# Performance work log

Measured on AMD Instinct MI355X. Metric: run time of the kernel, lower is better.

Reference implementation:

```python
import jax, jax.numpy as jnp
import numpy as np

NUM_TOPICS = 100
VOCAB = 8192
MC_N = 20
MD_N = 20
LAMBDA_D = 0.7
LAMBDA_A = 100.0
WARMUP_RATIO = 0.5
NUM_EPOCHS = 200


def setup_inputs() -> dict:
    key = jax.random.key(0)
    k1, k2 = jax.random.split(key)
    beta = jax.random.normal(k1, (NUM_TOPICS, VOCAB), dtype=jnp.float32)
    W = jax.random.uniform(k2, (VOCAB, VOCAB), dtype=jnp.float32)
    # fill_diagonal_(1) in __init__
    d = jnp.arange(VOCAB)
    W = W.at[d, d].set(1.0)
    return {"beta": beta, "coherence_weight": W, "epoch": 120}


def reference(beta, coherence_weight, epoch):
    K, V = beta.shape
    rows = jnp.arange(K)[:, None]

    # --- Mc: top-Mc_n mask -> additive -99999 on non-topk entries ---
    _, mc_idx = jax.lax.top_k(beta, MC_N)                      # [K, Mc_n]
    Mc = jnp.zeros_like(beta).at[rows, mc_idx].set(1.0)        # [K, V]
    Mc_add = (1.0 - Mc) * (-99999.0)

    # softmax over masked beta is detached in the original
    p = jax.lax.stop_gradient(jax.nn.softmax(beta + Mc_add, axis=1))
    M = p @ coherence_weight                                    # [K, V]

    # row-wise min-max normalize, then Wc = 1 - normalized
    m_min = jnp.min(M, axis=1, keepdims=True)
    m_max = jnp.max(M, axis=1, keepdims=True)
    Wc = 1.0 - (M - m_min) / (m_max - m_min)

    loss = 100.0 * jax.nn.softmax(beta, axis=1) ** 2 * Wc       # [K, V]

    # --- diversity mask Md (lambda_d > 0.5 branch) ---
    _, md_idx = jax.lax.top_k(beta, MD_N)
    Md_mask = jnp.zeros_like(beta).at[rows, md_idx].set(1.0)    # [K, V]
    # Md[t, v] = any other row has v in its top-Md_n
    col_sum = jnp.sum(Md_mask, axis=0)                          # [V]
    Md = (col_sum[None, :] - Md_mask) > 0                       # [K, V] bool

    pos = jnp.sum(jnp.where(Md, loss, 0.0))
    neg = jnp.sum(jnp.where(Md, 0.0, loss))
    total = (pos * LAMBDA_D + neg * (1.0 - LAMBDA_D)) * 2.0

    warmup_epochs = int(WARMUP_RATIO * NUM_EPOCHS)              # 100
    lambda_a_delta = LAMBDA_A / warmup_epochs
    lambda_a = epoch * lambda_a_delta if epoch < warmup_epochs else LAMBDA_A
    return lambda_a * total
```

## Files before the change

kernel.cpp:

```cpp
#include <hip/hip_runtime.h>
#include <math.h>

#define NT 100
#define VOCAB 8192
#define TOPN 20
#define CHUNKS 8
#define CCOLS (VOCAB / CHUNKS)
#define CAP 4096

__global__ __launch_bounds__(256) void topk_kernel(
    const float* __restrict__ beta,
    int*   __restrict__ top_idx,
    float* __restrict__ top_p,
    float* __restrict__ rowstats)
{
    const int k = blockIdx.x;
    const int t = threadIdx.x;

    __shared__ float srow[VOCAB];
    __shared__ float sred[4];
    __shared__ int   sredi[4];
    __shared__ float s_T;
    __shared__ int   s_base;
    __shared__ float cu[CAP];
    __shared__ unsigned short ci[CAP];
    __shared__ float s_winv[TOPN];
    __shared__ int   s_wini[TOPN];
    __shared__ float s_ps;

    const float* row = beta + (size_t)k * VOCAB;

    float mx = -INFINITY;
#pragma unroll
    for (int i = 0; i < VOCAB / (256 * 4); ++i) {
        float4 v = *reinterpret_cast<const float4*>(row + (size_t)(i * 256 + t) * 4);
        reinterpret_cast<float4*>(srow)[i * 256 + t] = v;
        mx = fmaxf(mx, fmaxf(fmaxf(v.x, v.y), fmaxf(v.z, v.w)));
    }
#pragma unroll
    for (int off = 32; off >= 1; off >>= 1) mx = fmaxf(mx, __shfl_down(mx, off));
    if ((t & 63) == 0) sred[t >> 6] = mx;
    __syncthreads();
    const float rowmax = fmaxf(fmaxf(sred[0], sred[1]), fmaxf(sred[2], sred[3]));

    float T = rowmax - 2.0f;
    for (int guard = 0; guard < 64; ++guard) {
        int c = 0;
#pragma unroll
        for (int i = 0; i < VOCAB / 256; ++i) c += (srow[i * 256 + t] >= T) ? 1 : 0;
#pragma unroll
        for (int off = 32; off >= 1; off >>= 1) c += __shfl_down(c, off);
        if ((t & 63) == 0) sredi[t >> 6] = c;
        __syncthreads();
        const int cnt = sredi[0] + sredi[1] + sredi[2] + sredi[3];
        if (cnt >= TOPN) { if (t == 0) s_T = T; break; }
        T -= 0.5f;
        __syncthreads();
    }
    if (t == 0) s_base = 0;
    __syncthreads();
    T = s_T;

#pragma unroll
    for (int i = 0; i < VOCAB / 256; ++i) {
        const int idx = i * 256 + t;
        const float v = srow[idx];
        const bool pr = (v >= T);
        const unsigned long long mask = __ballot(pr);
        const int lane = t & 63;
        const int pre = __popcll(mask & ((1ull << lane) - 1ull));
        const int nb  = __popcll(mask);
        int base = 0;
        if (lane == 0 && nb) base = atomicAdd(&s_base, nb);
        base = __shfl(base, 0);
        if (pr) {
            const int p = base + pre;
            if (p < CAP) { cu[p] = v; ci[p] = (unsigned short)idx; }
        }
    }
    __syncthreads();
    const int ncand = min(s_base, CAP);

    if (t < 64) {
        for (int it = 0; it < TOPN; ++it) {
            float bv = -INFINITY; int bp = -1;
            for (int p = t; p < ncand; p += 64) {
                const float v = cu[p];
                if (v > bv) { bv = v; bp = p; }
            }
#pragma unroll
            for (int off = 32; off >= 1; off >>= 1) {
                const float ov = __shfl_down(bv, off);
                const int   op = __shfl_down(bp, off);
                if (ov > bv) { bv = ov; bp = op; }
            }
            bp = __shfl(bp, 0);
            bv = __shfl(bv, 0);
            if (t == 0) { s_winv[it] = bv; s_wini[it] = ci[bp]; }
            cu[bp] = -INFINITY;
        }
    }
    __syncthreads();

    if (t == 0) {
        float ps = 0.f;
#pragma unroll
        for (int j = 0; j < TOPN; ++j) ps += expf(s_winv[j] - rowmax);
        s_ps = ps;
    }
    __syncthreads();
    if (t < TOPN) {
        top_idx[k * TOPN + t] = s_wini[t];
        top_p[k * TOPN + t]   = expf(s_winv[t] - rowmax) / s_ps;
    }

    float se = 0.f;
#pragma unroll
    for (int i = 0; i < VOCAB / 256; ++i) se += expf(srow[i * 256 + t] - rowmax);
#pragma unroll
    for (int off = 32; off >= 1; off >>= 1) se += __shfl_down(se, off);
    if ((t & 63) == 0) sred[t >> 6] = se;
    __syncthreads();
    if (t == 0) {
        rowstats[2 * k + 0] = rowmax;
        rowstats[2 * k + 1] = sred[0] + sred[1] + sred[2] + sred[3];
    }
}

__global__ __launch_bounds__(256) void mcompute_kernel(
    const float* __restrict__ W,
    const int*   __restrict__ top_idx,
    const float* __restrict__ top_p,
    float* __restrict__ M,
    float* __restrict__ mmpart)
{
    const int b = blockIdx.x;
    const int k = b / CHUNKS;
    const int c = b % CHUNKS;
    const int t = threadIdx.x;

    __shared__ int   sIdx[TOPN];
    __shared__ float sP[TOPN];
    __shared__ float sA[4], sB[4];
    if (t < TOPN) { sIdx[t] = top_idx[k * TOPN + t]; sP[t] = top_p[k * TOPN + t]; }
    __syncthreads();

    int   idx_r[TOPN];
    float p_r[TOPN];
#pragma unroll
    for (int j = 0; j < TOPN; ++j) { idx_r[j] = sIdx[j]; p_r[j] = sP[j]; }

    const int col = c * CCOLS + t * 4;
    float4 m = make_float4(0.f, 0.f, 0.f, 0.f);
#pragma unroll
    for (int j = 0; j < TOPN; ++j) {
        const float4 w = *reinterpret_cast<const float4*>(W + (size_t)idx_r[j] * VOCAB + col);
        const float pj = p_r[j];
        m.x += pj * w.x; m.y += pj * w.y; m.z += pj * w.z; m.w += pj * w.w;
    }
    *reinterpret_cast<float4*>(M + (size_t)k * VOCAB + col) = m;

    float mn = fminf(fminf(m.x, m.y), fminf(m.z, m.w));
    float mxv = fmaxf(fmaxf(m.x, m.y), fmaxf(m.z, m.w));
#pragma unroll
    for (int off = 32; off >= 1; off >>= 1) {
        mn  = fminf(mn,  __shfl_down(mn,  off));
        mxv = fmaxf(mxv, __shfl_down(mxv, off));
    }
    if ((t & 63) == 0) { sA[t >> 6] = mn; sB[t >> 6] = mxv; }
    __syncthreads();
    if (t == 0) {
        mmpart[(k * CHUNKS + c) * 2 + 0] = fminf(fminf(sA[0], sA[1]), fminf(sA[2], sA[3]));
        mmpart[(k * CHUNKS + c) * 2 + 1] = fmaxf(fmaxf(sB[0], sB[1]), fmaxf(sB[2], sB[3]));
    }
}

__global__ __launch_bounds__(1024) void loss_kernel(
    const float* __restrict__ beta,
    const float* __restrict__ M,
    const int*   __restrict__ top_idx,
    const float* __restrict__ rowstats,
    const float* __restrict__ mmpart,
    float* __restrict__ posk,
    float* __restrict__ negk)
{
    const int k = blockIdx.x;
    const int t = threadIdx.x;

    __shared__ int cnt[VOCAB];
    __shared__ float sredA[16], sredB[16];
    __shared__ float s_mn, s_mx;

#pragma unroll
    for (int i = 0; i < VOCAB / 1024; ++i) cnt[i * 1024 + t] = 0;
    __syncthreads();

    for (int e = t; e < NT * TOPN; e += 1024) atomicAdd(&cnt[top_idx[e]], 1);
    __syncthreads();
    if (t < TOPN) atomicSub(&cnt[top_idx[k * TOPN + t]], 1);
    if (t == 0) {
        float mn = INFINITY, mxv = -INFINITY;
        for (int c = 0; c < CHUNKS; ++c) {
            mn  = fminf(mn,  mmpart[(k * CHUNKS + c) * 2 + 0]);
            mxv = fmaxf(mxv, mmpart[(k * CHUNKS + c) * 2 + 1]);
        }
        s_mn = mn; s_mx = mxv;
    }
    __syncthreads();

    const float mmin = s_mn;
    const float inv  = 1.0f / (s_mx - mmin);
    const float rmax = rowstats[2 * k + 0];
    const float rinv = 1.0f / rowstats[2 * k + 1];

    float pos = 0.f, neg = 0.f;
#pragma unroll
    for (int i = 0; i < VOCAB / (1024 * 4); ++i) {
        const int v = (i * 1024 + t) * 4;
        const float4 m = *reinterpret_cast<const float4*>(M + (size_t)k * VOCAB + v);
        const float4 b = *reinterpret_cast<const float4*>(beta + (size_t)k * VOCAB + v);
        {
            const float Wc = 1.0f - (m.x - mmin) * inv;
            const float sb = expf(b.x - rmax) * rinv;
            const float l  = 100.f * sb * sb * Wc;
            if (cnt[v + 0] > 0) pos += l; else neg += l;
        }
        {
            const float Wc = 1.0f - (m.y - mmin) * inv;
            const float sb = expf(b.y - rmax) * rinv;
            const float l  = 100.f * sb * sb * Wc;
            if (cnt[v + 1] > 0) pos += l; else neg += l;
        }
        {
            const float Wc = 1.0f - (m.z - mmin) * inv;
            const float sb = expf(b.z - rmax) * rinv;
            const float l  = 100.f * sb * sb * Wc;
            if (cnt[v + 2] > 0) pos += l; else neg += l;
        }
        {
            const float Wc = 1.0f - (m.w - mmin) * inv;
            const float sb = expf(b.w - rmax) * rinv;
            const float l  = 100.f * sb * sb * Wc;
            if (cnt[v + 3] > 0) pos += l; else neg += l;
        }
    }
#pragma unroll
    for (int off = 32; off >= 1; off >>= 1) {
        pos += __shfl_down(pos, off);
        neg += __shfl_down(neg, off);
    }
    if ((t & 63) == 0) { sredA[t >> 6] = pos; sredB[t >> 6] = neg; }
    __syncthreads();
    if (t == 0) {
        float a = 0.f, b2 = 0.f;
        for (int w = 0; w < 16; ++w) { a += sredA[w]; b2 += sredB[w]; }
        posk[k] = a;
        negk[k] = b2;
    }
}

__global__ void finalize_kernel(const float* __restrict__ posk,
                                const float* __restrict__ negk,
                                const int*   __restrict__ epoch,
                                float* __restrict__ out)
{
    if (threadIdx.x == 0 && blockIdx.x == 0) {
        float pos = 0.f, neg = 0.f;
        for (int i = 0; i < NT; ++i) { pos += posk[i]; neg += negk[i]; }
        const float total = (pos * 0.7f + neg * 0.3f) * 2.0f;
        const int e = *epoch;
        const float la = (e < 100) ? (float)e : 100.0f;
        *out = la * total;
    }
}

extern "C" void kernel_launch(void* const* d_in, const int* in_sizes, int n_in,
                              void* d_out, int out_size, void* d_ws, size_t ws_size,
                              hipStream_t stream)
{
    (void)in_sizes; (void)n_in; (void)out_size; (void)ws_size;
    const float* beta  = (const float*)d_in[0];
    const float* W     = (const float*)d_in[1];
    const int*   epoch = (const int*)d_in[2];
    float* out = (float*)d_out;

    char* ws = (char*)d_ws;
    int*   top_idx  = (int*)ws;    ws += NT * TOPN * sizeof(int);
    float* top_p    = (float*)ws;  ws += NT * TOPN * sizeof(float);
    float* rowstats = (float*)ws;  ws += NT * 2 * sizeof(float);
    float* mmpart   = (float*)ws;  ws += NT * CHUNKS * 2 * sizeof(float);
    float* posk     = (float*)ws;  ws += NT * sizeof(float);
    float* negk     = (float*)ws;  ws += NT * sizeof(float);
    ws = (char*)(((size_t)ws + 255) & ~(size_t)255);
    float* M        = (float*)ws;  ws += (size_t)NT * VOCAB * sizeof(float);

    topk_kernel<<<NT, 256, 0, stream>>>(beta, top_idx, top_p, rowstats);
    mcompute_kernel<<<NT * CHUNKS, 256, 0, stream>>>(W, top_idx, top_p, M, mmpart);
    loss_kernel<<<NT, 1024, 0, stream>>>(beta, M, top_idx, rowstats, mmpart, posk, negk);
    finalize_kernel<<<1, 64, 0, stream>>>(posk, negk, epoch, out);
}
```

Baseline: 56.59 us.

## Fuse M computation with loss via algebraic min-max decomposition

The loss is expanded algebraically into per-chunk sums of w and w*M, so the M matrix never goes to global memory and the separate loss kernel is removed. The min-max normalization is applied later in the finalize kernel. The top-k kernel now keeps the beta row in registers instead of shared memory. This removes one launch and a 3.2MB write/read round trip, but each block now rebuilds a partial histogram of top indices, and the expanded form may lose some floating-point precision.

```diff
diff --git a/kernel.cpp b/kernel.cpp
--- a/kernel.cpp
+++ b/kernel.cpp
@@ -17,7 +17,6 @@
     const int k = blockIdx.x;
     const int t = threadIdx.x;
 
-    __shared__ float srow[VOCAB];
     __shared__ float sred[4];
     __shared__ int   sredi[4];
     __shared__ float s_T;
@@ -30,12 +29,12 @@
 
     const float* row = beta + (size_t)k * VOCAB;
 
+    float4 r[8];
     float mx = -INFINITY;
 #pragma unroll
-    for (int i = 0; i < VOCAB / (256 * 4); ++i) {
-        float4 v = *reinterpret_cast<const float4*>(row + (size_t)(i * 256 + t) * 4);
-        reinterpret_cast<float4*>(srow)[i * 256 + t] = v;
-        mx = fmaxf(mx, fmaxf(fmaxf(v.x, v.y), fmaxf(v.z, v.w)));
+    for (int i = 0; i < 8; ++i) {
+        r[i] = *reinterpret_cast<const float4*>(row + (size_t)(i * 256 + t) * 4);
+        mx = fmaxf(mx, fmaxf(fmaxf(r[i].x, r[i].y), fmaxf(r[i].z, r[i].w)));
     }
 #pragma unroll
     for (int off = 32; off >= 1; off >>= 1) mx = fmaxf(mx, __shfl_down(mx, off));
@@ -47,7 +46,12 @@
     for (int guard = 0; guard < 64; ++guard) {
         int c = 0;
 #pragma unroll
-        for (int i = 0; i < VOCAB / 256; ++i) c += (srow[i * 256 + t] >= T) ? 1 : 0;
+        for (int i = 0; i < 8; ++i) {
+            c += (r[i].x >= T) ? 1 : 0;
+            c += (r[i].y >= T) ? 1 : 0;
+            c += (r[i].z >= T) ? 1 : 0;
+            c += (r[i].w >= T) ? 1 : 0;
+        }
 #pragma unroll
         for (int off = 32; off >= 1; off >>= 1) c += __shfl_down(c, off);
         if ((t & 63) == 0) sredi[t >> 6] = c;
@@ -62,20 +66,22 @@
     T = s_T;
 
 #pragma unroll
-    for (int i = 0; i < VOCAB / 256; ++i) {
-        const int idx = i * 256 + t;
-        const float v = srow[idx];
-        const bool pr = (v >= T);
-        const unsigned long long mask = __ballot(pr);
-        const int lane = t & 63;
-        const int pre = __popcll(mask & ((1ull << lane) - 1ull));
-        const int nb  = __popcll(mask);
-        int base = 0;
-        if (lane == 0 && nb) base = atomicAdd(&s_base, nb);
-        base = __shfl(base, 0);
-        if (pr) {
-            const int p = base + pre;
-            if (p < CAP) { cu[p] = v; ci[p] = (unsigned short)idx; }
+    for (int i = 0; i < 8; ++i) {
+#pragma unroll
+        for (int e = 0; e < 4; ++e) {
+            const float v = (&r[i].x)[e];
+            const int idx = (i * 256 + t) * 4 + e;
+            const bool pr = (v >= T);
+            const unsigned long long mask = __ballot(pr);
+            const int lane = t & 63;
+            const int pre = __popcll(mask & ((1ull << lane) - 1ull));
+            int base = 0;
+            if (lane == 0) base = atomicAdd(&s_base, __popcll(mask));
+            base = __shfl(base, 0);
+            if (pr) {
+                const int p = base + pre;
+                if (p < CAP) { cu[p] = v; ci[p] = (unsigned short)idx; }
+            }
         }
     }
     __syncthreads();
@@ -116,7 +122,12 @@
 
     float se = 0.f;
 #pragma unroll
-    for (int i = 0; i < VOCAB / 256; ++i) se += expf(srow[i * 256 + t] - rowmax);
+    for (int i = 0; i < 8; ++i) {
+        se += expf(r[i].x - rowmax);
+        se += expf(r[i].y - rowmax);
+        se += expf(r[i].z - rowmax);
+        se += expf(r[i].w - rowmax);
+    }
 #pragma unroll
     for (int off = 32; off >= 1; off >>= 1) se += __shfl_down(se, off);
     if ((t & 63) == 0) sred[t >> 6] = se;
@@ -127,12 +138,14 @@
     }
 }
 
-__global__ __launch_bounds__(256) void mcompute_kernel(
+__global__ __launch_bounds__(256) void fused_kernel(
+    const float* __restrict__ beta,
     const float* __restrict__ W,
     const int*   __restrict__ top_idx,
     const float* __restrict__ top_p,
-    float* __restrict__ M,
-    float* __restrict__ mmpart)
+    const float* __restrict__ rowstats,
+    float* __restrict__ mmpart,
+    float* __restrict__ parts)
 {
     const int b = blockIdx.x;
     const int k = b / CHUNKS;
@@ -141,16 +154,31 @@
 
     __shared__ int   sIdx[TOPN];
     __shared__ float sP[TOPN];
-    __shared__ float sA[4], sB[4];
+    __shared__ int   cnt[CCOLS];
+    __shared__ float sA[4], sB[4], sC[4], sD[4], sE[4], sF[4];
+
     if (t < TOPN) { sIdx[t] = top_idx[k * TOPN + t]; sP[t] = top_p[k * TOPN + t]; }
-    __syncthreads();
+#pragma unroll
+    for (int i = 0; i < CCOLS / 256; ++i) cnt[i * 256 + t] = 0;
+    __syncthreads();
+
+    const int lo = c * CCOLS;
+    for (int e = t; e < NT * TOPN; e += 256) {
+        const int v = top_idx[e] - lo;
+        if ((unsigned)v < (unsigned)CCOLS) atomicAdd(&cnt[v], 1);
+    }
+    __syncthreads();
+    if (t < TOPN) {
+        const int v = sIdx[t] - lo;
+        if ((unsigned)v < (unsigned)CCOLS) atomicSub(&cnt[v], 1);
+    }
 
     int   idx_r[TOPN];
     float p_r[TOPN];
 #pragma unroll
     for (int j = 0; j < TOPN; ++j) { idx_r[j] = sIdx[j]; p_r[j] = sP[j]; }
 
-    const int col = c * CCOLS + t * 4;
+    const int col = lo + t * 4;
     float4 m = make_float4(0.f, 0.f, 0.f, 0.f);
 #pragma unroll
     for (int j = 0; j < TOPN; ++j) {
@@ -158,116 +186,87 @@
         const float pj = p_r[j];
         m.x += pj * w.x; m.y += pj * w.y; m.z += pj * w.z; m.w += pj * w.w;
     }
-    *reinterpret_cast<float4*>(M + (size_t)k * VOCAB + col) = m;
-
-    float mn = fminf(fminf(m.x, m.y), fminf(m.z, m.w));
+
+    float mn  = fminf(fminf(m.x, m.y), fminf(m.z, m.w));
     float mxv = fmaxf(fmaxf(m.x, m.y), fmaxf(m.z, m.w));
-#pragma unroll
-    for (int off = 32; off >= 1; off >>= 1) {
-        mn  = fminf(mn,  __shfl_down(mn,  off));
-        mxv = fmaxf(mxv, __shfl_down(mxv, off));
-    }
-    if ((t & 63) == 0) { sA[t >> 6] = mn; sB[t >> 6] = mxv; }
-    __syncthreads();
-    if (t == 0) {
-        mmpart[(k * CHUNKS + c) * 2 + 0] = fminf(fminf(sA[0], sA[1]), fminf(sA[2], sA[3]));
-        mmpart[(k * CHUNKS + c) * 2 + 1] = fmaxf(fmaxf(sB[0], sB[1]), fmaxf(sB[2], sB[3]));
-    }
-}
-
-__global__ __launch_bounds__(1024) void loss_kernel(
-    const float* __restrict__ beta,
-    const float* __restrict__ M,
-    const int*   __restrict__ top_idx,
-    const float* __restrict__ rowstats,
-    const float* __restrict__ mmpart,
-    float* __restrict__ posk,
-    float* __restrict__ negk)
-{
-    const int k = blockIdx.x;
-    const int t = threadIdx.x;
-
-    __shared__ int cnt[VOCAB];
-    __shared__ float sredA[16], sredB[16];
-    __shared__ float s_mn, s_mx;
-
-#pragma unroll
-    for (int i = 0; i < VOCAB / 1024; ++i) cnt[i * 1024 + t] = 0;
-    __syncthreads();
-
-    for (int e = t; e < NT * TOPN; e += 1024) atomicAdd(&cnt[top_idx[e]], 1);
-    __syncthreads();
-    if (t < TOPN) atomicSub(&cnt[top_idx[k * TOPN + t]], 1);
-    if (t == 0) {
-        float mn = INFINITY, mxv = -INFINITY;
-        for (int c = 0; c < CHUNKS; ++c) {
-            mn  = fminf(mn,  mmpart[(k * CHUNKS + c) * 2 + 0]);
-            mxv = fmaxf(mxv, mmpart[(k * CHUNKS + c) * 2 + 1]);
-        }
-        s_mn = mn; s_mx = mxv;
-    }
-    __syncthreads();
-
-    const float mmin = s_mn;
-    const float inv  = 1.0f / (s_mx - mmin);
+
     const float rmax = rowstats[2 * k + 0];
     const float rinv = 1.0f / rowstats[2 * k + 1];
-
+    const float4 bv = *reinterpret_cast<const float4*>(beta + (size_t)k * VOCAB + col);
+    float4 w4;
+    w4.x = expf(bv.x - rmax) * rinv;  w4.x = 100.f * w4.x * w4.x;
+    w4.y = expf(bv.y - rmax) * rinv;  w4.y = 100.f * w4.y * w4.y;
+    w4.z = expf(bv.z - rmax) * rinv;  w4.z = 100.f * w4.z * w4.z;
+    w4.w = expf(bv.w - rmax) * rinv;  w4.w = 100.f * w4.w * w4.w;
+
+    __syncthreads();
+
+    float Apos = 0.f, Bpos = 0.f, Aneg = 0.f, Bneg = 0.f;
+    {
+        const int lc = t * 4;
+        if (cnt[lc + 0] > 0) { Apos += w4.x; Bpos += w4.x * m.x; } else { Aneg += w4.x; Bneg += w4.x * m.x; }
+        if (cnt[lc + 1] > 0) { Apos += w4.y; Bpos += w4.y * m.y; } else { Aneg += w4.y; Bneg += w4.y * m.y; }
+        if (cnt[lc + 2] > 0) { Apos += w4.z; Bpos += w4.z * m.z; } else { Aneg += w4.z; Bneg += w4.z * m.z; }
+        if (cnt[lc + 3] > 0) { Apos += w4.w; Bpos += w4.w * m.w; } else { Aneg += w4.w; Bneg += w4.w * m.w; }
+    }
+
+#pragma unroll
+    for (int off = 32; off >= 1; off >>= 1) {
+        mn   = fminf(mn,  __shfl_down(mn,  off));
+        mxv  = fmaxf(mxv, __shfl_down(mxv, off));
+        Apos += __shfl_down(Apos, off);
+        Bpos += __shfl_down(Bpos, off);
+        Aneg += __shfl_down(Aneg, off);
+        Bneg += __shfl_down(Bneg, off);
+    }
+    if ((t & 63) == 0) {
+        const int w = t >> 6;
+        sA[w] = mn; sB[w] = mxv; sC[w] = Apos; sD[w] = Bpos; sE[w] = Aneg; sF[w] = Bneg;
+    }
+    __syncthreads();
+    if (t == 0) {
+        const int o = (k * CHUNKS + c);
+        mmpart[o * 2 + 0] = fminf(fminf(sA[0], sA[1]), fminf(sA[2], sA[3]));
+        mmpart[o * 2 + 1] = fmaxf(fmaxf(sB[0], sB[1]), fmaxf(sB[2], sB[3]));
+        parts[o * 4 + 0] = sC[0] + sC[1] + sC[2] + sC[3];
+        parts[o * 4 + 1] = sD[0] + sD[1] + sD[2] + sD[3];
+        parts[o * 4 + 2] = sE[0] + sE[1] + sE[2] + sE[3];
+        parts[o * 4 + 3] = sF[0] + sF[1] + sF[2] + sF[3];
+    }
+}
+
+__global__ __launch_bounds__(128) void finalize_kernel(
+    const float* __restrict__ mmpart,
+    const float* __restrict__ parts,
+    const int*   __restrict__ epoch,
+    float* __restrict__ out)
+{
+    const int t = threadIdx.x;
+    __shared__ float sp[128], sn[128];
     float pos = 0.f, neg = 0.f;
-#pragma unroll
-    for (int i = 0; i < VOCAB / (1024 * 4); ++i) {
-        const int v = (i * 1024 + t) * 4;
-        const float4 m = *reinterpret_cast<const float4*>(M + (size_t)k * VOCAB + v);
-        const float4 b = *reinterpret_cast<const float4*>(beta + (size_t)k * VOCAB + v);
-        {
-            const float Wc = 1.0f - (m.x - mmin) * inv;
-            const float sb = expf(b.x - rmax) * rinv;
-            const float l  = 100.f * sb * sb * Wc;
-            if (cnt[v + 0] > 0) pos += l; else neg += l;
-        }
-        {
-            const float Wc = 1.0f - (m.y - mmin) * inv;
-            const float sb = expf(b.y - rmax) * rinv;
-            const float l  = 100.f * sb * sb * Wc;
-            if (cnt[v + 1] > 0) pos += l; else neg += l;
-        }
-        {
-            const float Wc = 1.0f - (m.z - mmin) * inv;
-            const float sb = expf(b.z - rmax) * rinv;
-            const float l  = 100.f * sb * sb * Wc;
-            if (cnt[v + 2] > 0) pos += l; else neg += l;
-        }
-        {
-            const float Wc = 1.0f - (m.w - mmin) * inv;
-            const float sb = expf(b.w - rmax) * rinv;
-            const float l  = 100.f * sb * sb * Wc;
-            if (cnt[v + 3] > 0) pos += l; else neg += l;
-        }
-    }
-#pragma unroll
-    for (int off = 32; off >= 1; off >>= 1) {
-        pos += __shfl_down(pos, off);
-        neg += __shfl_down(neg, off);
-    }
-    if ((t & 63) == 0) { sredA[t >> 6] = pos; sredB[t >> 6] = neg; }
-    __syncthreads();
-    if (t == 0) {
-        float a = 0.f, b2 = 0.f;
-        for (int w = 0; w < 16; ++w) { a += sredA[w]; b2 += sredB[w]; }
-        posk[k] = a;
-        negk[k] = b2;
-    }
-}
-
-__global__ void finalize_kernel(const float* __restrict__ posk,
-                                const float* __restrict__ negk,
-                                const int*   __restrict__ epoch,
-                                float* __restrict__ out)
-{
-    if (threadIdx.x == 0 && blockIdx.x == 0) {
-        float pos = 0.f, neg = 0.f;
-        for (int i = 0; i < NT; ++i) { pos += posk[i]; neg += negk[i]; }
-        const float total = (pos * 0.7f + neg * 0.3f) * 2.0f;
+    if (t < NT) {
+        const int k = t;
+        float mn = INFINITY, mxv = -INFINITY;
+        float Apos = 0.f, Bpos = 0.f, Aneg = 0.f, Bneg = 0.f;
+        for (int c = 0; c < CHUNKS; ++c) {
+            const int o = k * CHUNKS + c;
+            mn  = fminf(mn,  mmpart[o * 2 + 0]);
+            mxv = fmaxf(mxv, mmpart[o * 2 + 1]);
+            Apos += parts[o * 4 + 0];
+            Bpos += parts[o * 4 + 1];
+            Aneg += parts[o * 4 + 2];
+            Bneg += parts[o * 4 + 3];
+        }
+        const float inv = 1.0f / (mxv - mn);
+        pos = Apos - inv * (Bpos - mn * Apos);
+        neg = Aneg - inv * (Bneg - mn * Aneg);
+    }
+    sp[t] = pos; sn[t] = neg;
+    __syncthreads();
+    if (t == 0) {
+        float P = 0.f, N = 0.f;
+        for (int i = 0; i < NT; ++i) { P += sp[i]; N += sn[i]; }
+        const float total = (P * 0.7f + N * 0.3f) * 2.0f;
         const int e = *epoch;
         const float la = (e < 100) ? (float)e : 100.0f;
         *out = la * total;
@@ -289,13 +288,9 @@
     float* top_p    = (float*)ws;  ws += NT * TOPN * sizeof(float);
     float* rowstats = (float*)ws;  ws += NT * 2 * sizeof(float);
     float* mmpart   = (float*)ws;  ws += NT * CHUNKS * 2 * sizeof(float);
-    float* posk     = (float*)ws;  ws += NT * sizeof(float);
-    float* negk     = (float*)ws;  ws += NT * sizeof(float);
-    ws = (char*)(((size_t)ws + 255) & ~(size_t)255);
-    float* M        = (float*)ws;  ws += (size_t)NT * VOCAB * sizeof(float);
+    float* parts    = (float*)ws;  ws += NT * CHUNKS * 4 * sizeof(float);
 
     topk_kernel<<<NT, 256, 0, stream>>>(beta, top_idx, top_p, rowstats);
-    mcompute_kernel<<<NT * CHUNKS, 256, 0, stream>>>(W, top_idx, top_p, M, mmpart);
-    loss_kernel<<<NT, 1024, 0, stream>>>(beta, M, top_idx, rowstats, mmpart, posk, negk);
-    finalize_kernel<<<1, 64, 0, stream>>>(posk, negk, epoch, out);
-}
+    fused_kernel<<<NT * CHUNKS, 256, 0, stream>>>(beta, W, top_idx, top_p, rowstats, mmpart, parts);
+    finalize_kernel<<<1, 128, 0, stream>>>(mmpart, parts, epoch, out);
+}
```

New measurement: 53.67 us. -5.2%, faster.
